# Kernel optimization log

Measured on AMD Instinct MI355X. Metric: run time of the kernel, lower is better.

The kernel has to match this reference:

```python
import jax, jax.numpy as jnp
import numpy as np

DIM = 768
N_HEADS = 12
HEAD_DIM = DIM // N_HEADS
MLP_MULT = 4
EPS = 1e-5


def setup_inputs() -> dict:
    key = jax.random.key(0)
    ks = jax.random.split(key, 8)
    B, T = 2, 4096
    s = lambda fan_in: 1.0 / np.sqrt(fan_in)
    return {
        "x": jax.random.normal(ks[0], (B, T, DIM), dtype=jnp.float32),
        "ln1_w": jnp.ones((DIM,), jnp.float32),
        "ln1_b": jnp.zeros((DIM,), jnp.float32),
        # weights stored as (in, out): y = x @ W + b (equivalent to torch Linear)
        "w_qkv": jax.random.normal(ks[1], (DIM, 3 * DIM), jnp.float32) * s(DIM),
        "w_proj": jax.random.normal(ks[2], (DIM, DIM), jnp.float32) * s(DIM),
        "b_proj": jnp.zeros((DIM,), jnp.float32),
        "ln2_w": jnp.ones((DIM,), jnp.float32),
        "ln2_b": jnp.zeros((DIM,), jnp.float32),
        "w1": jax.random.normal(ks[3], (DIM, MLP_MULT * DIM), jnp.float32) * s(DIM),
        "b1": jnp.zeros((MLP_MULT * DIM,), jnp.float32),
        "w2": jax.random.normal(ks[4], (MLP_MULT * DIM, DIM), jnp.float32) * s(MLP_MULT * DIM),
        "b2": jnp.zeros((DIM,), jnp.float32),
    }


def _layernorm(x, w, b):
    mean = jnp.mean(x, axis=-1, keepdims=True)
    var = jnp.var(x, axis=-1, keepdims=True)
    return w * (x - mean) * jax.lax.rsqrt(var + EPS) + b


def reference(x, ln1_w, ln1_b, w_qkv, w_proj, b_proj, ln2_w, ln2_b, w1, b1, w2, b2):
    B, T, C = x.shape
    scale = HEAD_DIM ** -0.5

    # --- attention sub-block (pre-LN) ---
    h = _layernorm(x, ln1_w, ln1_b)
    qkv = h @ w_qkv                               # [B, T, 3C]
    q, k, v = jnp.split(qkv, 3, axis=-1)
    to_heads = lambda t: t.reshape(B, T, N_HEADS, HEAD_DIM).transpose(0, 2, 1, 3)
    q, k, v = to_heads(q), to_heads(k), to_heads(v)  # [B, H, T, D]

    att = jnp.einsum("bhqd,bhkd->bhqk", q, k) * scale  # full T x T scores
    causal = jnp.tril(jnp.ones((T, T), dtype=bool))
    att = jnp.where(causal, att, -jnp.inf)
    att = jax.nn.softmax(att, axis=-1)
    y = jnp.einsum("bhqk,bhkd->bhqd", att, v)          # [B, H, T, D]
    y = y.transpose(0, 2, 1, 3).reshape(B, T, C)
    y = y @ w_proj + b_proj
    x = x + y

    # --- MLP sub-block (pre-LN) ---
    h = _layernorm(x, ln2_w, ln2_b)
    h = jax.nn.gelu(h @ w1 + b1, approximate=False)
    h = h @ w2 + b2
    return x + h
```

## Files before the change

kernel.cpp:

```cpp
#include <hip/hip_runtime.h>

typedef unsigned short u16;
typedef __attribute__((ext_vector_type(4))) unsigned short u16x4;
typedef __attribute__((ext_vector_type(8))) short short8;
typedef __attribute__((ext_vector_type(4))) float f32x4;
typedef __attribute__((ext_vector_type(16))) float f32x16;

#define MFMA32(a, b, c) __builtin_amdgcn_mfma_f32_32x32x16_bf16(a, b, c, 0, 0, 0)

__device__ __forceinline__ u16 f2bf(float f) {
  union { float f; unsigned u; } x; x.f = f;
  unsigned r = x.u + 0x7fffu + ((x.u >> 16) & 1u);
  return (u16)(r >> 16);
}

__device__ __forceinline__ unsigned cvt_pk_bf16(float lo, float hi) {
  unsigned r;
  asm("v_cvt_pk_bf16_f32 %0, %1, %2" : "=v"(r) : "v"(lo), "v"(hi));
  return r;
}

__device__ __forceinline__ void load_lds16(const void* g, void* l) {
  __builtin_amdgcn_global_load_lds(
      (const __attribute__((address_space(1))) void*)g,
      (__attribute__((address_space(3))) void*)l,
      16, 0, 0);
}

__global__ __launch_bounds__(256) void transpose_k(const float* __restrict__ in,
                                                   u16* __restrict__ out,
                                                   int R, int C) {
  __shared__ float tile[32][33];
  const int tx = threadIdx.x & 31, ty = threadIdx.x >> 5;
  const int c0 = blockIdx.x * 32, r0 = blockIdx.y * 32;
#pragma unroll
  for (int i = 0; i < 4; ++i)
    tile[ty + i * 8][tx] = in[(size_t)(r0 + ty + i * 8) * C + c0 + tx];
  __syncthreads();
#pragma unroll
  for (int i = 0; i < 4; ++i)
    out[(size_t)(c0 + ty + i * 8) * R + r0 + tx] = f2bf(tile[tx][ty + i * 8]);
}

__global__ __launch_bounds__(256) void ln_k(const float* __restrict__ X,
                                            const float* __restrict__ w,
                                            const float* __restrict__ b,
                                            u16* __restrict__ O) {
  const int row = blockIdx.x;
  const float* xr = X + (size_t)row * 768;
  const int tid = threadIdx.x;
  float v0 = xr[tid], v1 = xr[tid + 256], v2 = xr[tid + 512];
  float s = v0 + v1 + v2;
  float s2 = v0 * v0 + v1 * v1 + v2 * v2;
#pragma unroll
  for (int m = 32; m; m >>= 1) { s += __shfl_xor(s, m); s2 += __shfl_xor(s2, m); }
  __shared__ float ps[4], ps2[4];
  if ((tid & 63) == 0) { ps[tid >> 6] = s; ps2[tid >> 6] = s2; }
  __syncthreads();
  s = ps[0] + ps[1] + ps[2] + ps[3];
  s2 = ps2[0] + ps2[1] + ps2[2] + ps2[3];
  const float mean = s * (1.f / 768.f);
  const float var = s2 * (1.f / 768.f) - mean * mean;
  const float rstd = rsqrtf(var + 1e-5f);
  u16* orow = O + (size_t)row * 768;
  orow[tid]       = f2bf((v0 - mean) * rstd * w[tid]       + b[tid]);
  orow[tid + 256] = f2bf((v1 - mean) * rstd * w[tid + 256] + b[tid + 256]);
  orow[tid + 512] = f2bf((v2 - mean) * rstd * w[tid + 512] + b[tid + 512]);
}

#define BM 128
#define BN 128
#define BKK 64

template <int EPI>
__global__ __launch_bounds__(256, 2) void gemm_k(
    const u16* __restrict__ A, const u16* __restrict__ Bt, int K, int N,
    const float* __restrict__ bias, const float* __restrict__ res,
    float* __restrict__ outF, u16* __restrict__ outB,
    u16* __restrict__ qout, u16* __restrict__ kout, u16* __restrict__ vout) {
  __shared__ __align__(16) u16 sA[BM * BKK];
  __shared__ __align__(16) u16 sB[BN * BKK];
  const int nTn = N / BN;
  const int nwg = gridDim.x;
  const int bid = ((int)blockIdx.x & 7) * (nwg >> 3) + ((int)blockIdx.x >> 3);
  const int tm = bid / nTn, tn = bid % nTn;
  const int m0 = tm * BM, n0 = tn * BN;
  const int tid = threadIdx.x, lane = tid & 63, wv = tid >> 6;
  const int wr = wv >> 1, wc = wv & 1;
  const int fr = lane & 15, fg = lane >> 4;

  const u16* aSrc[4];
  const u16* bSrc[4];
#pragma unroll
  for (int i = 0; i < 4; ++i) {
    int f = (i * 4 + wv) * 64 + lane;
    int r = f >> 3;
    int c = (f & 7) ^ (r & 7);
    aSrc[i] = A + (size_t)(m0 + r) * K + c * 8;
    bSrc[i] = Bt + (size_t)(n0 + r) * K + c * 8;
  }

  f32x4 acc[4][4];
#pragma unroll
  for (int m = 0; m < 4; ++m)
#pragma unroll
    for (int n = 0; n < 4; ++n) acc[m][n] = f32x4{0.f, 0.f, 0.f, 0.f};

  const int aswz = fr & 7;
  for (int kt = 0; kt < K; kt += BKK) {
#pragma unroll
    for (int i = 0; i < 4; ++i) {
      load_lds16(aSrc[i] + kt, (char*)sA + (i * 4 + wv) * 1024);
      load_lds16(bSrc[i] + kt, (char*)sB + (i * 4 + wv) * 1024);
    }
    __syncthreads();
#pragma unroll
    for (int ks = 0; ks < 2; ++ks) {
      const int c16 = (ks * 4 + fg) ^ aswz;
      short8 af[4], bf[4];
#pragma unroll
      for (int m = 0; m < 4; ++m)
        af[m] = *(const short8*)((const char*)sA +
                                 (((wr * 64 + m * 16 + fr) * 8 + c16) << 4));
#pragma unroll
      for (int n = 0; n < 4; ++n)
        bf[n] = *(const short8*)((const char*)sB +
                                 (((wc * 64 + n * 16 + fr) * 8 + c16) << 4));
#pragma unroll
      for (int m = 0; m < 4; ++m)
#pragma unroll
        for (int n = 0; n < 4; ++n)
          acc[m][n] =
              __builtin_amdgcn_mfma_f32_16x16x32_bf16(af[m], bf[n], acc[m][n], 0, 0, 0);
    }
    __syncthreads();
  }

#pragma unroll
  for (int m = 0; m < 4; ++m) {
    const int row = m0 + wr * 64 + m * 16 + fg * 4;
#pragma unroll
    for (int n = 0; n < 4; ++n) {
      const int col = n0 + wc * 64 + n * 16 + fr;
      f32x4 v = acc[m][n];
      if (EPI == 0) {
        const int part = (col >= 1536) ? 2 : (col >= 768 ? 1 : 0);
        const int cc = col - part * 768;
        const int hh = cc >> 6, dd = cc & 63;
        const int bb = row >> 12;
        const int t = row & 4095;
        const size_t bhh = (size_t)(bb * 12 + hh);
        if (part == 2) {
          const int ks_ = (t & 63) >> 4, h_ = (t >> 3) & 1, e0 = t & 7;
          u16x4 pk = {f2bf(v[0]), f2bf(v[1]), f2bf(v[2]), f2bf(v[3])};
          *(u16x4*)(vout + bhh * 262144 + (size_t)(t >> 6) * 4096 +
                    (size_t)(((ks_ << 2) + ((dd >> 5) << 1) + h_) * 256 +
                             (dd & 31) * 8 + e0)) = pk;
        } else if (part == 1) {
          const int ks_ = dd >> 4, h_ = (dd >> 3) & 1, e = dd & 7;
          u16* base = kout + bhh * 262144;
#pragma unroll
          for (int r = 0; r < 4; ++r) {
            const int t2 = t + r;
            base[(size_t)(t2 >> 6) * 4096 +
                 (size_t)((((ks_ << 2) + (((t2 & 63) >> 5) << 1) + h_) * 256) +
                          (t2 & 31) * 8 + e)] = f2bf(v[r]);
          }
        } else {
          const float qs = 0.18033688011112042f;
          u16* dst = qout + (bhh * 4096 + t) * 64 + dd;
#pragma unroll
          for (int r = 0; r < 4; ++r) dst[(size_t)r * 64] = f2bf(v[r] * qs);
        }
      } else if (EPI == 1) {
        const float bv = bias[col];
#pragma unroll
        for (int r = 0; r < 4; ++r)
          outF[(size_t)(row + r) * N + col] =
              v[r] + bv + res[(size_t)(row + r) * N + col];
      } else {
        const float bv = bias[col];
#pragma unroll
        for (int r = 0; r < 4; ++r) {
          float t = v[r] + bv;
          float g = 0.5f * t * (1.f + erff(t * 0.70710678118654752f));
          outB[(size_t)(row + r) * N + col] = f2bf(g);
        }
      }
    }
  }
}

__global__ __launch_bounds__(256) void attn_k(const u16* __restrict__ Q,
                                              const u16* __restrict__ Kb,
                                              const u16* __restrict__ Vt,
                                              u16* __restrict__ Y) {
  __shared__ __align__(16) u16 sK[2][8192];
  __shared__ __align__(16) u16 sV[2][8192];
  const int bid = blockIdx.x;
  const int qt = 31 - bid / 24;
  const int bh = bid % 24;
  const int bb = bh / 12, hh = bh - bb * 12;
  const int tid = threadIdx.x, lane = tid & 63, wv = tid >> 6;
  const int l31 = lane & 31, hi = lane >> 5;
  const int wq0 = qt * 128 + wv * 32;
  const int qG = wq0 + l31;
  const u16* Qh = Q + (size_t)bh * 4096 * 64;
  const u16* Kh = Kb + (size_t)bh * 262144;
  const u16* Vh = Vt + (size_t)bh * 262144;

  short8 qf[4];
#pragma unroll
  for (int ks = 0; ks < 4; ++ks)
    qf[ks] = *(const short8*)(Qh + (size_t)qG * 64 + ks * 16 + hi * 8);

  f32x16 yacc[2];
  yacc[0] = (f32x16)0.f;
  yacc[1] = (f32x16)0.f;
  float lrun = 0.f;

#define STAGE(buf, cc)                                                         \
  do {                                                                         \
    const u16* gk_ = Kh + (size_t)(cc)*8192;                                   \
    const u16* gv_ = Vh + (size_t)(cc)*8192;                                   \
    _Pragma("unroll") for (int i_ = 0; i_ < 4; ++i_) {                         \
      const int f_ = i_ * 256 + tid;                                           \
      load_lds16(gk_ + f_ * 8, (char*)sK[buf] + f_ * 16);                      \
      load_lds16(gv_ + f_ * 8, (char*)sV[buf] + f_ * 16);                      \
    }                                                                          \
  } while (0)

  const int nch = qt + 1;
  STAGE(0, 0);
  __syncthreads();

  const int rdBase = hi * 512 + l31 * 16;

  for (int c = 0; c < nch; ++c) {
    const int cur = c & 1;
    if (c + 1 < nch) STAGE(cur ^ 1, c + 1);

#pragma unroll
    for (int hf = 0; hf < 2; ++hf) {
      const int kb = c * 128 + hf * 64;
      if (kb <= wq0 + 31) {
        const char* sKb = (const char*)sK[cur] + hf * 8192;
        const char* sVb = (const char*)sV[cur] + hf * 8192;

        f32x16 s[2];
        s[0] = (f32x16)0.f;
        s[1] = (f32x16)0.f;
        __builtin_amdgcn_s_setprio(1);
#pragma unroll
        for (int ks = 0; ks < 4; ++ks) {
#pragma unroll
          for (int kc = 0; kc < 2; ++kc) {
            short8 kf = *(const short8*)(sKb + ks * 2048 + kc * 1024 + rdBase);
            s[kc] = MFMA32(kf, qf[ks], s[kc]);
          }
        }
        __builtin_amdgcn_s_setprio(0);

        if (kb + 63 > wq0) {
#pragma unroll
          for (int kc = 0; kc < 2; ++kc)
#pragma unroll
            for (int r = 0; r < 16; ++r) {
              const int key = kb + kc * 32 + (r & 3) + 8 * (r >> 2) + 4 * hi;
              if (key > qG) s[kc][r] = -3e38f;
            }
        }

#pragma unroll
        for (int kc = 0; kc < 2; ++kc)
#pragma unroll
          for (int r = 0; r < 16; ++r)
            s[kc][r] = __builtin_amdgcn_exp2f(s[kc][r] - 8.f);

        float u[8];
#pragma unroll
        for (int i = 0; i < 8; ++i)
          u[i] = (s[0][i] + s[0][i + 8]) + (s[1][i] + s[1][i + 8]);
#pragma unroll
        for (int st = 4; st; st >>= 1)
#pragma unroll
          for (int i = 0; i < st; ++i) u[i] += u[i + st];
        lrun += u[0] + __shfl_xor(u[0], 32);

#pragma unroll
        for (int ks2 = 0; ks2 < 4; ++ks2) {
          const int kc = ks2 >> 1, rb = (ks2 & 1) * 8;
          unsigned W0 = cvt_pk_bf16(s[kc][rb + 0], s[kc][rb + 1]);
          unsigned W1 = cvt_pk_bf16(s[kc][rb + 2], s[kc][rb + 3]);
          unsigned W2 = cvt_pk_bf16(s[kc][rb + 4], s[kc][rb + 5]);
          unsigned W3 = cvt_pk_bf16(s[kc][rb + 6], s[kc][rb + 7]);
          asm("v_permlane32_swap_b32 %0, %1" : "+v"(W0), "+v"(W2));
          asm("v_permlane32_swap_b32 %0, %1" : "+v"(W1), "+v"(W3));
          union { unsigned w[4]; short8 v; } pb;
          pb.w[0] = W0; pb.w[1] = W1; pb.w[2] = W2; pb.w[3] = W3;
          __builtin_amdgcn_s_setprio(1);
#pragma unroll
          for (int dt = 0; dt < 2; ++dt) {
            short8 vf = *(const short8*)(sVb + ks2 * 2048 + dt * 1024 + rdBase);
            yacc[dt] = MFMA32(vf, pb.v, yacc[dt]);
          }
          __builtin_amdgcn_s_setprio(0);
        }
      }
    }
    __syncthreads();
  }

  const float inv = 1.f / lrun;
  u16* Yr = Y + (size_t)(bb * 4096 + qt * 128 + wv * 32 + l31) * 768 + hh * 64;
#pragma unroll
  for (int dt = 0; dt < 2; ++dt)
#pragma unroll
    for (int g = 0; g < 4; ++g) {
      u16x4 pk = {f2bf(yacc[dt][g * 4 + 0] * inv), f2bf(yacc[dt][g * 4 + 1] * inv),
                  f2bf(yacc[dt][g * 4 + 2] * inv), f2bf(yacc[dt][g * 4 + 3] * inv)};
      *(u16x4*)(Yr + dt * 32 + g * 8 + hi * 4) = pk;
    }
}

extern "C" void kernel_launch(void* const* d_in, const int* in_sizes, int n_in,
                              void* d_out, int out_size, void* d_ws, size_t ws_size,
                              hipStream_t stream) {
  const float* x = (const float*)d_in[0];
  const float* ln1w = (const float*)d_in[1];
  const float* ln1b = (const float*)d_in[2];
  const float* wqkv = (const float*)d_in[3];
  const float* wproj = (const float*)d_in[4];
  const float* bproj = (const float*)d_in[5];
  const float* ln2w = (const float*)d_in[6];
  const float* ln2b = (const float*)d_in[7];
  const float* w1 = (const float*)d_in[8];
  const float* b1 = (const float*)d_in[9];
  const float* w2 = (const float*)d_in[10];
  const float* b2 = (const float*)d_in[11];
  float* out = (float*)d_out;
  char* ws = (char*)d_ws;

  const size_t SZ_ACT = (size_t)8192 * 768 * 2;
  u16* hbuf = (u16*)(ws);
  u16* qb = (u16*)(ws + SZ_ACT);
  u16* kb = (u16*)(ws + 2 * SZ_ACT);
  u16* vT = (u16*)(ws + 3 * SZ_ACT);
  u16* ybuf = (u16*)(ws + 4 * SZ_ACT);
  float* out1 = (float*)(ws + 5 * SZ_ACT);
  char* wsw = ws + 5 * SZ_ACT + (size_t)8192 * 768 * 4;
  u16* wqkvT = (u16*)(wsw);
  u16* wprojT = (u16*)(wsw + 3538944);
  u16* w1T = (u16*)(wsw + 3538944 + 1179648);
  u16* w2T = (u16*)(wsw + 3538944 + 1179648 + 4718592);
  u16* h3 = hbuf;
  u16* h2 = ybuf;

  transpose_k<<<dim3(2304 / 32, 768 / 32), 256, 0, stream>>>(wqkv, wqkvT, 768, 2304);
  transpose_k<<<dim3(768 / 32, 768 / 32), 256, 0, stream>>>(wproj, wprojT, 768, 768);
  transpose_k<<<dim3(3072 / 32, 768 / 32), 256, 0, stream>>>(w1, w1T, 768, 3072);
  transpose_k<<<dim3(768 / 32, 3072 / 32), 256, 0, stream>>>(w2, w2T, 3072, 768);

  ln_k<<<8192, 256, 0, stream>>>(x, ln1w, ln1b, hbuf);

  gemm_k<0><<<64 * (2304 / 128), 256, 0, stream>>>(hbuf, wqkvT, 768, 2304,
      nullptr, nullptr, nullptr, nullptr, qb, kb, vT);

  attn_k<<<768, 256, 0, stream>>>(qb, kb, vT, ybuf);

  gemm_k<1><<<64 * (768 / 128), 256, 0, stream>>>(ybuf, wprojT, 768, 768,
      bproj, x, out1, nullptr, nullptr, nullptr, nullptr);

  ln_k<<<8192, 256, 0, stream>>>(out1, ln2w, ln2b, h2);

  gemm_k<2><<<64 * (3072 / 128), 256, 0, stream>>>(h2, w1T, 768, 3072,
      b1, nullptr, nullptr, h3, nullptr, nullptr, nullptr);

  gemm_k<1><<<64 * (768 / 128), 256, 0, stream>>>(h3, w2T, 3072, 768,
      b2, out1, out, nullptr, nullptr, nullptr, nullptr);

  (void)in_sizes; (void)n_in; (void)out_size; (void)ws_size;
}
```

Before: 279.8 us.

## Make attention kernel persistent with atomic work-queue scheduling

The attention kernel becomes persistent: 512 blocks repeatedly grab (q-tile, batch-head) work items from a global atomic counter, heaviest causal tiles first, instead of launching one block per item. The goal is better load balance across compute units for the triangular causal workload and less tail imbalance. It costs an extra memset launch to reset the counter, one atomic and barrier per item, and relies on the hardware dispatch pattern leaving two resident blocks per CU.

```diff
diff --git a/kernel.cpp b/kernel.cpp
--- a/kernel.cpp
+++ b/kernel.cpp
@@ -194,35 +194,19 @@
 __global__ __launch_bounds__(256) void attn_k(const u16* __restrict__ Q,
                                               const u16* __restrict__ Kb,
                                               const u16* __restrict__ Vt,
-                                              u16* __restrict__ Y) {
+                                              u16* __restrict__ Y,
+                                              int* __restrict__ cnt) {
   __shared__ __align__(16) u16 sK[2][8192];
   __shared__ __align__(16) u16 sV[2][8192];
-  const int bid = blockIdx.x;
-  const int qt = 31 - bid / 24;
-  const int bh = bid % 24;
-  const int bb = bh / 12, hh = bh - bb * 12;
+  __shared__ int s_item;
   const int tid = threadIdx.x, lane = tid & 63, wv = tid >> 6;
   const int l31 = lane & 31, hi = lane >> 5;
-  const int wq0 = qt * 128 + wv * 32;
-  const int qG = wq0 + l31;
-  const u16* Qh = Q + (size_t)bh * 4096 * 64;
-  const u16* Kh = Kb + (size_t)bh * 262144;
-  const u16* Vh = Vt + (size_t)bh * 262144;
-
-  short8 qf[4];
-#pragma unroll
-  for (int ks = 0; ks < 4; ++ks)
-    qf[ks] = *(const short8*)(Qh + (size_t)qG * 64 + ks * 16 + hi * 8);
-
-  f32x16 yacc[2];
-  yacc[0] = (f32x16)0.f;
-  yacc[1] = (f32x16)0.f;
-  float lrun = 0.f;
-
-#define STAGE(buf, cc)                                                         \
+  const int rdBase = hi * 512 + l31 * 16;
+
+#define STAGE(buf, cc, Kh_, Vh_)                                               \
   do {                                                                         \
-    const u16* gk_ = Kh + (size_t)(cc)*8192;                                   \
-    const u16* gv_ = Vh + (size_t)(cc)*8192;                                   \
+    const u16* gk_ = (Kh_) + (size_t)(cc)*8192;                                \
+    const u16* gv_ = (Vh_) + (size_t)(cc)*8192;                                \
     _Pragma("unroll") for (int i_ = 0; i_ < 4; ++i_) {                         \
       const int f_ = i_ * 256 + tid;                                           \
       load_lds16(gk_ + f_ * 8, (char*)sK[buf] + f_ * 16);                      \
@@ -230,97 +214,121 @@
     }                                                                          \
   } while (0)
 
-  const int nch = qt + 1;
-  STAGE(0, 0);
-  __syncthreads();
-
-  const int rdBase = hi * 512 + l31 * 16;
-
-  for (int c = 0; c < nch; ++c) {
-    const int cur = c & 1;
-    if (c + 1 < nch) STAGE(cur ^ 1, c + 1);
-
-#pragma unroll
-    for (int hf = 0; hf < 2; ++hf) {
-      const int kb = c * 128 + hf * 64;
-      if (kb <= wq0 + 31) {
-        const char* sKb = (const char*)sK[cur] + hf * 8192;
-        const char* sVb = (const char*)sV[cur] + hf * 8192;
-
-        f32x16 s[2];
-        s[0] = (f32x16)0.f;
-        s[1] = (f32x16)0.f;
-        __builtin_amdgcn_s_setprio(1);
-#pragma unroll
-        for (int ks = 0; ks < 4; ++ks) {
-#pragma unroll
-          for (int kc = 0; kc < 2; ++kc) {
-            short8 kf = *(const short8*)(sKb + ks * 2048 + kc * 1024 + rdBase);
-            s[kc] = MFMA32(kf, qf[ks], s[kc]);
+  for (;;) {
+    if (tid == 0) s_item = atomicAdd(cnt, 1);
+    __syncthreads();
+    const int it = s_item;
+    if (it >= 768) return;
+    const int qt = 31 - it / 24;
+    const int bh = it % 24;
+    const int bb = bh / 12, hh = bh - bb * 12;
+    const int wq0 = qt * 128 + wv * 32;
+    const int qG = wq0 + l31;
+    const u16* Qh = Q + (size_t)bh * 4096 * 64;
+    const u16* Kh = Kb + (size_t)bh * 262144;
+    const u16* Vh = Vt + (size_t)bh * 262144;
+
+    short8 qf[4];
+#pragma unroll
+    for (int ks = 0; ks < 4; ++ks)
+      qf[ks] = *(const short8*)(Qh + (size_t)qG * 64 + ks * 16 + hi * 8);
+
+    f32x16 yacc[2];
+    yacc[0] = (f32x16)0.f;
+    yacc[1] = (f32x16)0.f;
+    float lrun = 0.f;
+
+    const int nch = qt + 1;
+    STAGE(0, 0, Kh, Vh);
+    __syncthreads();
+
+    for (int c = 0; c < nch; ++c) {
+      const int cur = c & 1;
+      if (c + 1 < nch) STAGE(cur ^ 1, c + 1, Kh, Vh);
+
+#pragma unroll
+      for (int hf = 0; hf < 2; ++hf) {
+        const int kb = c * 128 + hf * 64;
+        if (kb <= wq0 + 31) {
+          const char* sKb = (const char*)sK[cur] + hf * 8192;
+          const char* sVb = (const char*)sV[cur] + hf * 8192;
+
+          f32x16 s[2];
+          s[0] = (f32x16)0.f;
+          s[1] = (f32x16)0.f;
+          __builtin_amdgcn_s_setprio(1);
+#pragma unroll
+          for (int ks = 0; ks < 4; ++ks) {
+#pragma unroll
+            for (int kc = 0; kc < 2; ++kc) {
+              short8 kf = *(const short8*)(sKb + ks * 2048 + kc * 1024 + rdBase);
+              s[kc] = MFMA32(kf, qf[ks], s[kc]);
+            }
+          }
+          __builtin_amdgcn_s_setprio(0);
+
+          if (kb + 63 > wq0) {
+#pragma unroll
+            for (int kc = 0; kc < 2; ++kc)
+#pragma unroll
+              for (int r = 0; r < 16; ++r) {
+                const int key = kb + kc * 32 + (r & 3) + 8 * (r >> 2) + 4 * hi;
+                if (key > qG) s[kc][r] = -3e38f;
+              }
+          }
+
+#pragma unroll
+          for (int kc = 0; kc < 2; ++kc)
+#pragma unroll
+            for (int r = 0; r < 16; ++r)
+              s[kc][r] = __builtin_amdgcn_exp2f(s[kc][r] - 8.f);
+
+          float u[8];
+#pragma unroll
+          for (int i = 0; i < 8; ++i)
+            u[i] = (s[0][i] + s[0][i + 8]) + (s[1][i] + s[1][i + 8]);
+#pragma unroll
+          for (int st = 4; st; st >>= 1)
+#pragma unroll
+            for (int i = 0; i < st; ++i) u[i] += u[i + st];
+          lrun += u[0] + __shfl_xor(u[0], 32);
+
+#pragma unroll
+          for (int ks2 = 0; ks2 < 4; ++ks2) {
+            const int kc = ks2 >> 1, rb = (ks2 & 1) * 8;
+            unsigned W0 = cvt_pk_bf16(s[kc][rb + 0], s[kc][rb + 1]);
+            unsigned W1 = cvt_pk_bf16(s[kc][rb + 2], s[kc][rb + 3]);
+            unsigned W2 = cvt_pk_bf16(s[kc][rb + 4], s[kc][rb + 5]);
+            unsigned W3 = cvt_pk_bf16(s[kc][rb + 6], s[kc][rb + 7]);
+            asm("v_permlane32_swap_b32 %0, %1" : "+v"(W0), "+v"(W2));
+            asm("v_permlane32_swap_b32 %0, %1" : "+v"(W1), "+v"(W3));
+            union { unsigned w[4]; short8 v; } pb;
+            pb.w[0] = W0; pb.w[1] = W1; pb.w[2] = W2; pb.w[3] = W3;
+            __builtin_amdgcn_s_setprio(1);
+#pragma unroll
+            for (int dt = 0; dt < 2; ++dt) {
+              short8 vf = *(const short8*)(sVb + ks2 * 2048 + dt * 1024 + rdBase);
+              yacc[dt] = MFMA32(vf, pb.v, yacc[dt]);
+            }
+            __builtin_amdgcn_s_setprio(0);
           }
         }
-        __builtin_amdgcn_s_setprio(0);
-
-        if (kb + 63 > wq0) {
-#pragma unroll
-          for (int kc = 0; kc < 2; ++kc)
-#pragma unroll
-            for (int r = 0; r < 16; ++r) {
-              const int key = kb + kc * 32 + (r & 3) + 8 * (r >> 2) + 4 * hi;
-              if (key > qG) s[kc][r] = -3e38f;
-            }
-        }
-
-#pragma unroll
-        for (int kc = 0; kc < 2; ++kc)
-#pragma unroll
-          for (int r = 0; r < 16; ++r)
-            s[kc][r] = __builtin_amdgcn_exp2f(s[kc][r] - 8.f);
-
-        float u[8];
-#pragma unroll
-        for (int i = 0; i < 8; ++i)
-          u[i] = (s[0][i] + s[0][i + 8]) + (s[1][i] + s[1][i + 8]);
-#pragma unroll
-        for (int st = 4; st; st >>= 1)
-#pragma unroll
-          for (int i = 0; i < st; ++i) u[i] += u[i + st];
-        lrun += u[0] + __shfl_xor(u[0], 32);
-
-#pragma unroll
-        for (int ks2 = 0; ks2 < 4; ++ks2) {
-          const int kc = ks2 >> 1, rb = (ks2 & 1) * 8;
-          unsigned W0 = cvt_pk_bf16(s[kc][rb + 0], s[kc][rb + 1]);
-          unsigned W1 = cvt_pk_bf16(s[kc][rb + 2], s[kc][rb + 3]);
-          unsigned W2 = cvt_pk_bf16(s[kc][rb + 4], s[kc][rb + 5]);
-          unsigned W3 = cvt_pk_bf16(s[kc][rb + 6], s[kc][rb + 7]);
-          asm("v_permlane32_swap_b32 %0, %1" : "+v"(W0), "+v"(W2));
-          asm("v_permlane32_swap_b32 %0, %1" : "+v"(W1), "+v"(W3));
-          union { unsigned w[4]; short8 v; } pb;
-          pb.w[0] = W0; pb.w[1] = W1; pb.w[2] = W2; pb.w[3] = W3;
-          __builtin_amdgcn_s_setprio(1);
-#pragma unroll
-          for (int dt = 0; dt < 2; ++dt) {
-            short8 vf = *(const short8*)(sVb + ks2 * 2048 + dt * 1024 + rdBase);
-            yacc[dt] = MFMA32(vf, pb.v, yacc[dt]);
-          }
-          __builtin_amdgcn_s_setprio(0);
-        }
       }
+      __syncthreads();
     }
-    __syncthreads();
+
+    const float inv = 1.f / lrun;
+    u16* Yr = Y + (size_t)(bb * 4096 + qt * 128 + wv * 32 + l31) * 768 + hh * 64;
+#pragma unroll
+    for (int dt = 0; dt < 2; ++dt)
+#pragma unroll
+      for (int g = 0; g < 4; ++g) {
+        u16x4 pk = {f2bf(yacc[dt][g * 4 + 0] * inv), f2bf(yacc[dt][g * 4 + 1] * inv),
+                    f2bf(yacc[dt][g * 4 + 2] * inv), f2bf(yacc[dt][g * 4 + 3] * inv)};
+        *(u16x4*)(Yr + dt * 32 + g * 8 + hi * 4) = pk;
+      }
   }
-
-  const float inv = 1.f / lrun;
-  u16* Yr = Y + (size_t)(bb * 4096 + qt * 128 + wv * 32 + l31) * 768 + hh * 64;
-#pragma unroll
-  for (int dt = 0; dt < 2; ++dt)
-#pragma unroll
-    for (int g = 0; g < 4; ++g) {
-      u16x4 pk = {f2bf(yacc[dt][g * 4 + 0] * inv), f2bf(yacc[dt][g * 4 + 1] * inv),
-                  f2bf(yacc[dt][g * 4 + 2] * inv), f2bf(yacc[dt][g * 4 + 3] * inv)};
-      *(u16x4*)(Yr + dt * 32 + g * 8 + hi * 4) = pk;
-    }
+#undef STAGE
 }
 
 extern "C" void kernel_launch(void* const* d_in, const int* in_sizes, int n_in,
@@ -353,6 +361,7 @@
   u16* wprojT = (u16*)(wsw + 3538944);
   u16* w1T = (u16*)(wsw + 3538944 + 1179648);
   u16* w2T = (u16*)(wsw + 3538944 + 1179648 + 4718592);
+  int* cnt = (int*)(wsw + 3538944 + 1179648 + 4718592 + 4718592);
   u16* h3 = hbuf;
   u16* h2 = ybuf;
 
@@ -366,7 +375,8 @@
   gemm_k<0><<<64 * (2304 / 128), 256, 0, stream>>>(hbuf, wqkvT, 768, 2304,
       nullptr, nullptr, nullptr, nullptr, qb, kb, vT);
 
-  attn_k<<<768, 256, 0, stream>>>(qb, kb, vT, ybuf);
+  hipMemsetAsync(cnt, 0, 4, stream);
+  attn_k<<<512, 256, 0, stream>>>(qb, kb, vT, ybuf, cnt);
 
   gemm_k<1><<<64 * (768 / 128), 256, 0, stream>>>(ybuf, wprojT, 768, 768,
       bproj, x, out1, nullptr, nullptr, nullptr, nullptr);
```

Result: slower. 302.7 us (+8.2%).

## Use 128x64-tile GEMM kernel for N=768 projections to fill more CUs

Applied to the files above, without the earlier changes.

Adds a new GEMM kernel with 128x64 output tiles, 16x16x32 MFMA, XOR-swizzled LDS and an XCD-aware block remap. It replaces the 128x128 gemm_k for the two N=768 projection GEMMs (attention proj and MLP down). The aim is to double the workgroup count from 384 to 768 so the 256 CUs are better occupied. In exchange it uses single-buffered LDS with a sync on every k-step, so load latency is not overlapped, and each B tile is reused less.

```diff
diff --git a/kernel.cpp b/kernel.cpp
--- a/kernel.cpp
+++ b/kernel.cpp
@@ -191,6 +191,90 @@
   }
 }
 
+__global__ __launch_bounds__(256, 2) void gemm64_k(
+    const u16* __restrict__ A, const u16* __restrict__ Bt, int K, int N,
+    const float* __restrict__ bias, const float* __restrict__ res,
+    float* __restrict__ outF) {
+  __shared__ __align__(16) u16 sA[128 * 64];
+  __shared__ __align__(16) u16 sB[64 * 64];
+  const int nTn = N / 64;
+  const int nwg = gridDim.x;
+  const int bid = ((int)blockIdx.x & 7) * (nwg >> 3) + ((int)blockIdx.x >> 3);
+  const int tm = bid / nTn, tn = bid % nTn;
+  const int m0 = tm * 128, n0 = tn * 64;
+  const int tid = threadIdx.x, lane = tid & 63, wv = tid >> 6;
+  const int fr = lane & 15, fg = lane >> 4;
+
+  const u16* aSrc[4];
+  const u16* bSrc[2];
+#pragma unroll
+  for (int i = 0; i < 4; ++i) {
+    const int f = i * 256 + tid;
+    const int r = f >> 3;
+    const int c = (f & 7) ^ (r & 7);
+    aSrc[i] = A + (size_t)(m0 + r) * K + c * 8;
+  }
+#pragma unroll
+  for (int i = 0; i < 2; ++i) {
+    const int f = i * 256 + tid;
+    const int r = f >> 3;
+    const int c = (f & 7) ^ (r & 7);
+    bSrc[i] = Bt + (size_t)(n0 + r) * K + c * 8;
+  }
+
+  f32x4 acc[2][4];
+#pragma unroll
+  for (int m = 0; m < 2; ++m)
+#pragma unroll
+    for (int n = 0; n < 4; ++n) acc[m][n] = f32x4{0.f, 0.f, 0.f, 0.f};
+
+  const int aswz = fr & 7;
+  for (int kt = 0; kt < K; kt += 64) {
+#pragma unroll
+    for (int i = 0; i < 4; ++i)
+      load_lds16(aSrc[i] + kt, (char*)sA + (i * 256 + tid) * 16);
+#pragma unroll
+    for (int i = 0; i < 2; ++i)
+      load_lds16(bSrc[i] + kt, (char*)sB + (i * 256 + tid) * 16);
+    __syncthreads();
+#pragma unroll
+    for (int ks = 0; ks < 2; ++ks) {
+      const int c16 = (ks * 4 + fg) ^ aswz;
+      short8 af[2], bf[4];
+#pragma unroll
+      for (int m = 0; m < 2; ++m)
+        af[m] = *(const short8*)((const char*)sA +
+                                 (((wv * 32 + m * 16 + fr) * 8 + c16) << 4));
+#pragma unroll
+      for (int n = 0; n < 4; ++n)
+        bf[n] = *(const short8*)((const char*)sB +
+                                 (((n * 16 + fr) * 8 + c16) << 4));
+#pragma unroll
+      for (int m = 0; m < 2; ++m)
+#pragma unroll
+        for (int n = 0; n < 4; ++n)
+          acc[m][n] =
+              __builtin_amdgcn_mfma_f32_16x16x32_bf16(af[m], bf[n], acc[m][n], 0, 0, 0);
+    }
+    __syncthreads();
+  }
+
+#pragma unroll
+  for (int m = 0; m < 2; ++m) {
+    const int row = m0 + wv * 32 + m * 16 + fg * 4;
+#pragma unroll
+    for (int n = 0; n < 4; ++n) {
+      const int col = n0 + n * 16 + fr;
+      const float bv = bias[col];
+      f32x4 v = acc[m][n];
+#pragma unroll
+      for (int r = 0; r < 4; ++r)
+        outF[(size_t)(row + r) * N + col] =
+            v[r] + bv + res[(size_t)(row + r) * N + col];
+    }
+  }
+}
+
 __global__ __launch_bounds__(256) void attn_k(const u16* __restrict__ Q,
                                               const u16* __restrict__ Kb,
                                               const u16* __restrict__ Vt,
@@ -321,6 +405,7 @@
                   f2bf(yacc[dt][g * 4 + 2] * inv), f2bf(yacc[dt][g * 4 + 3] * inv)};
       *(u16x4*)(Yr + dt * 32 + g * 8 + hi * 4) = pk;
     }
+#undef STAGE
 }
 
 extern "C" void kernel_launch(void* const* d_in, const int* in_sizes, int n_in,
@@ -368,16 +453,16 @@
 
   attn_k<<<768, 256, 0, stream>>>(qb, kb, vT, ybuf);
 
-  gemm_k<1><<<64 * (768 / 128), 256, 0, stream>>>(ybuf, wprojT, 768, 768,
-      bproj, x, out1, nullptr, nullptr, nullptr, nullptr);
+  gemm64_k<<<64 * (768 / 64), 256, 0, stream>>>(ybuf, wprojT, 768, 768,
+      bproj, x, out1);
 
   ln_k<<<8192, 256, 0, stream>>>(out1, ln2w, ln2b, h2);
 
   gemm_k<2><<<64 * (3072 / 128), 256, 0, stream>>>(h2, w1T, 768, 3072,
       b1, nullptr, nullptr, h3, nullptr, nullptr, nullptr);
 
-  gemm_k<1><<<64 * (768 / 128), 256, 0, stream>>>(h3, w2T, 3072, 768,
-      b2, out1, out, nullptr, nullptr, nullptr, nullptr);
+  gemm64_k<<<64 * (768 / 64), 256, 0, stream>>>(h3, w2T, 3072, 768,
+      b2, out1, out);
 
   (void)in_sizes; (void)n_in; (void)out_size; (void)ws_size;
 }
```

Result: faster. 272.1 us (-2.8%).
